# Kernel tuning notes

Hardware: AMD Instinct MI355X
Metric: run time of the kernel (lower is better)

The kernel has to match this reference:

```python
import jax, jax.numpy as jnp
import numpy as np

HIDDEN = 4096
N_HEADS = 32
N_KV_HEADS = 8
HEAD_DIM = HIDDEN // N_HEADS  # 128
B, S = 2, 4096


def setup_inputs() -> dict:
    key = jax.random.key(0)
    ks = jax.random.split(key, 9)
    sc = 1.0 / np.sqrt(HIDDEN)
    x = jax.random.normal(ks[0], (B, S, HIDDEN), dtype=jnp.float32)
    Wq = jax.random.normal(ks[1], (HIDDEN, HIDDEN), dtype=jnp.float32) * sc
    bq = jax.random.normal(ks[2], (HIDDEN,), dtype=jnp.float32) * 0.01
    Wk = jax.random.normal(ks[3], (N_KV_HEADS * HEAD_DIM, HIDDEN), dtype=jnp.float32) * sc
    bk = jax.random.normal(ks[4], (N_KV_HEADS * HEAD_DIM,), dtype=jnp.float32) * 0.01
    Wv = jax.random.normal(ks[5], (N_KV_HEADS * HEAD_DIM, HIDDEN), dtype=jnp.float32) * sc
    bv = jax.random.normal(ks[6], (N_KV_HEADS * HEAD_DIM,), dtype=jnp.float32) * 0.01
    Wo = jax.random.normal(ks[7], (HIDDEN, HIDDEN), dtype=jnp.float32) * sc
    bo = jax.random.normal(ks[8], (HIDDEN,), dtype=jnp.float32) * 0.01
    return {"x": x, "Wq": Wq, "bq": bq, "Wk": Wk, "bk": bk,
            "Wv": Wv, "bv": bv, "Wo": Wo, "bo": bo}


def reference(x, Wq, bq, Wk, bk, Wv, bv, Wo, bo):
    batch, seq, _ = x.shape
    # Linear projections (torch Linear: x @ W^T + b)
    q = x @ Wq.T + bq                      # [B,S,H*D]
    k = x @ Wk.T + bk                      # [B,S,Hkv*D]
    v = x @ Wv.T + bv
    q = q.reshape(batch, seq, N_HEADS, HEAD_DIM)
    k = k.reshape(batch, seq, N_KV_HEADS, HEAD_DIM)
    v = v.reshape(batch, seq, N_KV_HEADS, HEAD_DIM)
    # GQA handling in source: concatenate [k]*r along head axis (a TILE, not interleave)
    r = N_HEADS // N_KV_HEADS
    k = jnp.tile(k, (1, 1, r, 1))          # [B,S,H,D]
    v = jnp.tile(v, (1, 1, r, 1))
    # Source keeps layout [B,S,H,D]; mx.matmul batches over (B,S), so
    # attention is taken ACROSS THE HEAD AXIS per token (faithful to source).
    scores = jnp.einsum('bshd,bsgd->bshg', q, k) / np.sqrt(HEAD_DIM)  # [B,S,H,H]
    weights = jax.nn.softmax(scores, axis=-1)
    attn = jnp.einsum('bshg,bsgd->bshd', weights, v)  # [B,S,H,D]
    attn = attn.reshape(batch, seq, HIDDEN)
    return attn @ Wo.T + bo
```

## Files before the change

kernel.cpp:

```cpp
#include <hip/hip_runtime.h>
#include <hip/hip_bf16.h>


typedef _Float16 half8 __attribute__((ext_vector_type(8)));
typedef _Float16 half4v __attribute__((ext_vector_type(4)));
typedef float floatx4 __attribute__((ext_vector_type(4)));

#define K_DIM 4096
#define LDAB 8192
#define BM 256
#define BN 256
#define BK 32
#define NSTEP 128

__device__ __forceinline__ void gload16(const void* g, void* l) {
    __builtin_amdgcn_global_load_lds((const __attribute__((address_space(1))) void*)g,
                                     (__attribute__((address_space(3))) void*)l,
                                     16, 0, 0);
}

__global__ __launch_bounds__(256) void split_f32(
    const float* __restrict__ src, _Float16* __restrict__ dst, long long rows) {
    long long n4 = rows * 1024;
    long long stride = (long long)gridDim.x * blockDim.x;
    for (long long i = (long long)blockIdx.x * blockDim.x + threadIdx.x; i < n4; i += stride) {
        float4 v = ((const float4*)src)[i];
        long long r = i >> 10;
        int c = ((int)(i & 1023)) << 2;
        half4v hi, lo;
        hi[0] = (_Float16)v.x; lo[0] = (_Float16)(v.x - (float)hi[0]);
        hi[1] = (_Float16)v.y; lo[1] = (_Float16)(v.y - (float)hi[1]);
        hi[2] = (_Float16)v.z; lo[2] = (_Float16)(v.z - (float)hi[2]);
        hi[3] = (_Float16)v.w; lo[3] = (_Float16)(v.w - (float)hi[3]);
        *(half4v*)&dst[r * LDAB + c] = hi;
        *(half4v*)&dst[r * LDAB + K_DIM + c] = lo;
    }
}

__global__ __launch_bounds__(512, 2) void gemm_split3_8w(
    const _Float16* __restrict__ A, const _Float16* __restrict__ B,
    float* __restrict__ C, const float* __restrict__ bias0,
    const float* __restrict__ bias1, int N) {

    __shared__ __attribute__((aligned(16))) _Float16 lA[2][2][BM * BK];
    __shared__ __attribute__((aligned(16))) _Float16 lB[2][2][BN * BK];

    const int tid = threadIdx.x;
    const int lane = tid & 63;
    const int w = tid >> 6;
    const int wm = w >> 2;
    const int wn = w & 3;

    const int f = blockIdx.x;
    const int nwg = gridDim.x;
    const int lid = (f & 7) * (nwg >> 3) + (f >> 3);
    const long long brow = (long long)(lid & 31) * BM;
    const long long bcol = (long long)(lid >> 5) * BN;

    floatx4 acc[8][4];
#pragma unroll
    for (int m = 0; m < 8; ++m)
#pragma unroll
        for (int n = 0; n < 4; ++n)
            acc[m][n] = (floatx4){0.f, 0.f, 0.f, 0.f};

    const int srow = w * 16 + (lane >> 2);
    const int scol = 8 * ((lane & 3) ^ ((lane >> 3) & 3));
    const _Float16* Asrc = A + (brow + srow) * (long long)LDAB + scol;
    const _Float16* Bsrc = B + (bcol + srow) * (long long)LDAB + scol;

    const int rA = lane & 15;
    const int kcs = 8 * ((lane >> 4) ^ ((lane >> 1) & 3));

    auto stageA = [&](int NXT, int ktn) {
        gload16(Asrc + ktn, &lA[NXT][0][w * 512]);
        gload16(Asrc + 128 * (long long)LDAB + ktn, &lA[NXT][0][4096 + w * 512]);
        gload16(Asrc + K_DIM + ktn, &lA[NXT][1][w * 512]);
        gload16(Asrc + 128 * (long long)LDAB + K_DIM + ktn, &lA[NXT][1][4096 + w * 512]);
    };
    auto stageB = [&](int NXT, int ktn) {
        gload16(Bsrc + ktn, &lB[NXT][0][w * 512]);
        gload16(Bsrc + 128 * (long long)LDAB + ktn, &lB[NXT][0][4096 + w * 512]);
        gload16(Bsrc + K_DIM + ktn, &lB[NXT][1][w * 512]);
        gload16(Bsrc + 128 * (long long)LDAB + K_DIM + ktn, &lB[NXT][1][4096 + w * 512]);
    };

    stageA(0, 0);
    stageB(0, 0);
    asm volatile("s_waitcnt vmcnt(0)" ::: "memory");
    __builtin_amdgcn_s_barrier();

    auto step = [&](int CUR, int NXT, int ktn) {
        half8 ah[8], bh[4];
#pragma unroll
        for (int n = 0; n < 4; ++n)
            bh[n] = *(const half8*)&lB[CUR][0][(wn * 64 + n * 16 + rA) * BK + kcs];
#pragma unroll
        for (int m = 0; m < 8; ++m)
            ah[m] = *(const half8*)&lA[CUR][0][(wm * 128 + m * 16 + rA) * BK + kcs];
        stageA(NXT, ktn);
        __builtin_amdgcn_s_barrier();
        __builtin_amdgcn_s_setprio(1);
#pragma unroll
        for (int m = 0; m < 8; ++m)
#pragma unroll
            for (int n = 0; n < 4; ++n)
                acc[m][n] = __builtin_amdgcn_mfma_f32_16x16x32_f16(
                    ah[m], bh[n], acc[m][n], 0, 0, 0);
        __builtin_amdgcn_s_setprio(0);
        __builtin_amdgcn_s_barrier();
        {
            half8 bl[4];
#pragma unroll
            for (int n = 0; n < 4; ++n)
                bl[n] = *(const half8*)&lB[CUR][1][(wn * 64 + n * 16 + rA) * BK + kcs];
            stageB(NXT, ktn);
            __builtin_amdgcn_s_barrier();
            __builtin_amdgcn_s_setprio(1);
#pragma unroll
            for (int m = 0; m < 8; ++m)
#pragma unroll
                for (int n = 0; n < 4; ++n)
                    acc[m][n] = __builtin_amdgcn_mfma_f32_16x16x32_f16(
                        ah[m], bl[n], acc[m][n], 0, 0, 0);
            __builtin_amdgcn_s_setprio(0);
            __builtin_amdgcn_s_barrier();
        }
        {
            half8 al[8];
#pragma unroll
            for (int m = 0; m < 8; ++m)
                al[m] = *(const half8*)&lA[CUR][1][(wm * 128 + m * 16 + rA) * BK + kcs];
            __builtin_amdgcn_s_barrier();
            __builtin_amdgcn_s_setprio(1);
#pragma unroll
            for (int m = 0; m < 8; ++m)
#pragma unroll
                for (int n = 0; n < 4; ++n)
                    acc[m][n] = __builtin_amdgcn_mfma_f32_16x16x32_f16(
                        al[m], bh[n], acc[m][n], 0, 0, 0);
            __builtin_amdgcn_s_setprio(0);
            asm volatile("s_waitcnt vmcnt(0)" ::: "memory");
            __builtin_amdgcn_s_barrier();
        }
    };

    for (int tt = 0; tt < NSTEP; tt += 2) {
        step(0, 1, (tt + 1) * BK);
        step(1, 0, ((tt + 2) & (NSTEP - 1)) * BK);
    }

    const float* bias = (bias1 != nullptr && bcol >= 1024) ? (bias1 - 1024) : bias0;
    const int crow0 = (lane >> 4) * 4;
    const int ccol = lane & 15;
#pragma unroll
    for (int n = 0; n < 4; ++n) {
        long long col = bcol + wn * 64 + n * 16 + ccol;
        float bv_ = bias[col];
#pragma unroll
        for (int m = 0; m < 8; ++m) {
            long long row = brow + wm * 128 + m * 16 + crow0;
            float* cp = C + row * (long long)N + col;
            cp[0]             = acc[m][n][0] + bv_;
            cp[(long long)N]  = acc[m][n][1] + bv_;
            cp[2LL * N]       = acc[m][n][2] + bv_;
            cp[3LL * N]       = acc[m][n][3] + bv_;
        }
    }
}

__global__ __launch_bounds__(256) void attn_token(
    const float* __restrict__ q, const float* __restrict__ kv,
    _Float16* __restrict__ out) {

    const int token = blockIdx.x;
    __shared__ float sQ[32 * 128];
    __shared__ float sK[8 * 128];
    __shared__ float sV[8 * 128];
    __shared__ float sP[32 * 8];

    const int t = threadIdx.x;
    {
        const float4* gq = (const float4*)(q + (long long)token * 4096);
        float4* dq = (float4*)sQ;
        dq[t] = gq[t];
        dq[t + 256] = gq[t + 256];
        dq[t + 512] = gq[t + 512];
        dq[t + 768] = gq[t + 768];
        const float4* gkv = (const float4*)(kv + (long long)token * 2048);
        ((float4*)sK)[t] = gkv[t];
        ((float4*)sV)[t] = gkv[t + 256];
    }
    __syncthreads();

    const int h = t >> 3, j = t & 7;
    const float* qr = sQ + h * 128;
    const float* kr = sK + j * 128;
    float s = 0.f;
#pragma unroll
    for (int i = 0; i < 128; i += 4)
        s += qr[i] * kr[i] + qr[i + 1] * kr[i + 1] +
             qr[i + 2] * kr[i + 2] + qr[i + 3] * kr[i + 3];
    s *= 0.08838834764831845f;

    float mx = s;
    mx = fmaxf(mx, __shfl_xor(mx, 1, 8));
    mx = fmaxf(mx, __shfl_xor(mx, 2, 8));
    mx = fmaxf(mx, __shfl_xor(mx, 4, 8));
    float e = expf(s - mx);
    float sum = e;
    sum += __shfl_xor(sum, 1, 8);
    sum += __shfl_xor(sum, 2, 8);
    sum += __shfl_xor(sum, 4, 8);
    sP[t] = e / sum;
    __syncthreads();

    float p[8];
#pragma unroll
    for (int jj = 0; jj < 8; ++jj) p[jj] = sP[(t >> 3) * 8 + jj];
    const int d0 = (t & 7) * 16;
    const long long obase = (long long)token * LDAB + (t >> 3) * 128;
#pragma unroll
    for (int dd = 0; dd < 16; ++dd) {
        int d = d0 + dd;
        float a = 0.f;
#pragma unroll
        for (int jj = 0; jj < 8; ++jj) a += p[jj] * sV[jj * 128 + d];
        _Float16 hi = (_Float16)a;
        _Float16 lo = (_Float16)(a - (float)hi);
        out[obase + d] = hi;
        out[obase + K_DIM + d] = lo;
    }
}

extern "C" void kernel_launch(void* const* d_in, const int* in_sizes, int n_in,
                              void* d_out, int out_size, void* d_ws, size_t ws_size,
                              hipStream_t stream) {
    const float* x  = (const float*)d_in[0];
    const float* Wq = (const float*)d_in[1];
    const float* bq = (const float*)d_in[2];
    const float* Wk = (const float*)d_in[3];
    const float* bk = (const float*)d_in[4];
    const float* Wv = (const float*)d_in[5];
    const float* bv = (const float*)d_in[6];
    const float* Wo = (const float*)d_in[7];
    const float* bo = (const float*)d_in[8];
    float* out = (float*)d_out;

    char* ws = (char*)d_ws;
    _Float16* A2x  = (_Float16*)(ws + 0);
    _Float16* B2q  = (_Float16*)(ws + 134217728LL);
    _Float16* B2kv = (_Float16*)(ws + 201326592LL);
    _Float16* B2v  = (_Float16*)(ws + 218103808LL);
    _Float16* B2o  = (_Float16*)(ws + 234881024LL);
    float*    qb   = (float*)(ws + 301989888LL);
    float*    kvb  = (float*)(ws + 436207616LL);

    split_f32<<<2048, 256, 0, stream>>>(x,  A2x, 8192);
    split_f32<<<2048, 256, 0, stream>>>(Wq, B2q, 4096);
    split_f32<<<1024, 256, 0, stream>>>(Wk, B2kv, 1024);
    split_f32<<<1024, 256, 0, stream>>>(Wv, B2v, 1024);
    split_f32<<<2048, 256, 0, stream>>>(Wo, B2o, 4096);

    gemm_split3_8w<<<512, 512, 0, stream>>>(A2x, B2q,  qb,  bq, nullptr, 4096);
    gemm_split3_8w<<<256, 512, 0, stream>>>(A2x, B2kv, kvb, bk, bv,      2048);

    attn_token<<<8192, 256, 0, stream>>>(qb, kvb, A2x);

    gemm_split3_8w<<<512, 512, 0, stream>>>(A2x, B2o, out, bo, nullptr, 4096);
}
```

Before: 2.630 ms.

## Pipeline GEMM global-to-LDS loads in three groups with partial vmcnt waits

Splits the per-step prefetch into three load groups issued right after each LDS fragment read. Each sub-phase now waits with a partial vmcnt count plus one barrier, instead of draining all loads with vmcnt(0) at the end of every step. This is meant to overlap global loads with MFMA work and cut the number of barriers per step. The epilogue stores also become nontemporal. The partial-wait counts must exactly match the issue order, or LDS buffers could be read before their data arrives.

Result: faster. 2.432 ms (-7.5%).

```diff
diff --git a/kernel.cpp b/kernel.cpp
--- a/kernel.cpp
+++ b/kernel.cpp
@@ -72,34 +72,36 @@
     const int rA = lane & 15;
     const int kcs = 8 * ((lane >> 4) ^ ((lane >> 1) & 3));
 
-    auto stageA = [&](int NXT, int ktn) {
+    auto stageG1 = [&](int NXT, int ktn) {
         gload16(Asrc + ktn, &lA[NXT][0][w * 512]);
         gload16(Asrc + 128 * (long long)LDAB + ktn, &lA[NXT][0][4096 + w * 512]);
+        gload16(Bsrc + ktn, &lB[NXT][0][w * 512]);
+        gload16(Bsrc + 128 * (long long)LDAB + ktn, &lB[NXT][0][4096 + w * 512]);
+    };
+    auto stageG2 = [&](int NXT, int ktn) {
+        gload16(Bsrc + K_DIM + ktn, &lB[NXT][1][w * 512]);
+        gload16(Bsrc + 128 * (long long)LDAB + K_DIM + ktn, &lB[NXT][1][4096 + w * 512]);
+    };
+    auto stageG3 = [&](int NXT, int ktn) {
         gload16(Asrc + K_DIM + ktn, &lA[NXT][1][w * 512]);
         gload16(Asrc + 128 * (long long)LDAB + K_DIM + ktn, &lA[NXT][1][4096 + w * 512]);
     };
-    auto stageB = [&](int NXT, int ktn) {
-        gload16(Bsrc + ktn, &lB[NXT][0][w * 512]);
-        gload16(Bsrc + 128 * (long long)LDAB + ktn, &lB[NXT][0][4096 + w * 512]);
-        gload16(Bsrc + K_DIM + ktn, &lB[NXT][1][w * 512]);
-        gload16(Bsrc + 128 * (long long)LDAB + K_DIM + ktn, &lB[NXT][1][4096 + w * 512]);
-    };
-
-    stageA(0, 0);
-    stageB(0, 0);
-    asm volatile("s_waitcnt vmcnt(0)" ::: "memory");
-    __builtin_amdgcn_s_barrier();
+
+    stageG1(0, 0);
+    stageG2(0, 0);
+    stageG3(0, 0);
 
     auto step = [&](int CUR, int NXT, int ktn) {
         half8 ah[8], bh[4];
+        asm volatile("s_waitcnt vmcnt(4)" ::: "memory");
+        __builtin_amdgcn_s_barrier();
 #pragma unroll
         for (int n = 0; n < 4; ++n)
             bh[n] = *(const half8*)&lB[CUR][0][(wn * 64 + n * 16 + rA) * BK + kcs];
 #pragma unroll
         for (int m = 0; m < 8; ++m)
             ah[m] = *(const half8*)&lA[CUR][0][(wm * 128 + m * 16 + rA) * BK + kcs];
-        stageA(NXT, ktn);
-        __builtin_amdgcn_s_barrier();
+        stageG1(NXT, ktn);
         __builtin_amdgcn_s_setprio(1);
 #pragma unroll
         for (int m = 0; m < 8; ++m)
@@ -108,14 +110,14 @@
                 acc[m][n] = __builtin_amdgcn_mfma_f32_16x16x32_f16(
                     ah[m], bh[n], acc[m][n], 0, 0, 0);
         __builtin_amdgcn_s_setprio(0);
-        __builtin_amdgcn_s_barrier();
         {
             half8 bl[4];
+            asm volatile("s_waitcnt vmcnt(6)" ::: "memory");
+            __builtin_amdgcn_s_barrier();
 #pragma unroll
             for (int n = 0; n < 4; ++n)
                 bl[n] = *(const half8*)&lB[CUR][1][(wn * 64 + n * 16 + rA) * BK + kcs];
-            stageB(NXT, ktn);
-            __builtin_amdgcn_s_barrier();
+            stageG2(NXT, ktn);
             __builtin_amdgcn_s_setprio(1);
 #pragma unroll
             for (int m = 0; m < 8; ++m)
@@ -124,14 +126,15 @@
                     acc[m][n] = __builtin_amdgcn_mfma_f32_16x16x32_f16(
                         ah[m], bl[n], acc[m][n], 0, 0, 0);
             __builtin_amdgcn_s_setprio(0);
-            __builtin_amdgcn_s_barrier();
         }
         {
             half8 al[8];
+            asm volatile("s_waitcnt vmcnt(6)" ::: "memory");
+            __builtin_amdgcn_s_barrier();
 #pragma unroll
             for (int m = 0; m < 8; ++m)
                 al[m] = *(const half8*)&lA[CUR][1][(wm * 128 + m * 16 + rA) * BK + kcs];
-            __builtin_amdgcn_s_barrier();
+            stageG3(NXT, ktn);
             __builtin_amdgcn_s_setprio(1);
 #pragma unroll
             for (int m = 0; m < 8; ++m)
@@ -140,8 +143,6 @@
                     acc[m][n] = __builtin_amdgcn_mfma_f32_16x16x32_f16(
                         al[m], bh[n], acc[m][n], 0, 0, 0);
             __builtin_amdgcn_s_setprio(0);
-            asm volatile("s_waitcnt vmcnt(0)" ::: "memory");
-            __builtin_amdgcn_s_barrier();
         }
     };
 
@@ -149,6 +150,7 @@
         step(0, 1, (tt + 1) * BK);
         step(1, 0, ((tt + 2) & (NSTEP - 1)) * BK);
     }
+    asm volatile("s_waitcnt vmcnt(0)" ::: "memory");
 
     const float* bias = (bias1 != nullptr && bcol >= 1024) ? (bias1 - 1024) : bias0;
     const int crow0 = (lane >> 4) * 4;
@@ -161,10 +163,10 @@
         for (int m = 0; m < 8; ++m) {
             long long row = brow + wm * 128 + m * 16 + crow0;
             float* cp = C + row * (long long)N + col;
-            cp[0]             = acc[m][n][0] + bv_;
-            cp[(long long)N]  = acc[m][n][1] + bv_;
-            cp[2LL * N]       = acc[m][n][2] + bv_;
-            cp[3LL * N]       = acc[m][n][3] + bv_;
+            __builtin_nontemporal_store(acc[m][n][0] + bv_, cp);
+            __builtin_nontemporal_store(acc[m][n][1] + bv_, cp + (long long)N);
+            __builtin_nontemporal_store(acc[m][n][2] + bv_, cp + 2LL * N);
+            __builtin_nontemporal_store(acc[m][n][3] + bv_, cp + 3LL * N);
         }
     }
 }
```
